# Kernel optimization log

Measured on AMD Instinct MI355X. Metric: run time of the kernel, lower is better.

## Reference

```python
import jax, jax.numpy as jnp
import numpy as np

K = 3  # from init kwarg


def setup_inputs() -> dict:
    key = jax.random.key(0)
    k1, k2 = jax.random.split(key)
    B, N, D = 32, 2048, 128
    features = jax.random.normal(k1, (B, N, D), dtype=jnp.float32)
    strength = jax.random.uniform(k2, (), dtype=jnp.float32)
    return {"features": features, "strength": strength}


def reference(features, strength):
    B, N, D = features.shape
    k = min(K, N - 1)
    x = jax.lax.stop_gradient(features)  # torch uses features.detach() for the mix path

    # pairwise euclidean distance (torch.cdist, p=2): ||a||^2 + ||b||^2 - 2 a.b
    sq = jnp.sum(x * x, axis=-1)                     # (B, N)
    d2 = sq[:, :, None] + sq[:, None, :] - 2.0 * jnp.einsum('bnd,bmd->bnm', x, x)
    dist = jnp.sqrt(jnp.maximum(d2, 0.0))            # (B, N, N)

    # mask self-distance with +1e6 on the diagonal
    eye = jnp.eye(N, dtype=dist.dtype)
    dist = dist + eye[None, :, :] * 1000000.0

    # k smallest -> top_k of negated distances
    _, idx = jax.lax.top_k(-dist, k)                 # idx: (B, N, k)

    # gather neighbor features: gathered[b,n,j] = x[b, idx[b,n,j]]
    gathered = x[jnp.arange(B)[:, None, None], idx]  # (B, N, k, D)
    mix = jnp.mean(gathered, axis=2)                 # (B, N, D)

    s = jnp.clip(strength, 0.0, 1.0)
    return (1.0 - s) * features + s * mix
```

## Files before the change

kernel.cpp:

```cpp
#include <hip/hip_runtime.h>
#include <cfloat>

#define BB 32
#define NN 2048
#define DD 128
#define RM 64
#define CN 64

typedef __attribute__((ext_vector_type(8))) short short8;
typedef __attribute__((ext_vector_type(4))) float float4v;

__device__ __forceinline__ unsigned short f2bf(float f) {
    unsigned int u = __builtin_bit_cast(unsigned int, f);
    u += 0x7FFFu + ((u >> 16) & 1u);
    return (unsigned short)(u >> 16);
}

__device__ __forceinline__ unsigned int umn(unsigned int a, unsigned int b) { return a < b ? a : b; }
__device__ __forceinline__ unsigned int umx(unsigned int a, unsigned int b) { return a > b ? a : b; }
#define CSU(a, b) { unsigned int _lo = umn(a, b), _hi = umx(a, b); (a) = _lo; (b) = _hi; }

__device__ __forceinline__ void gl2lds16(const unsigned short* g, unsigned short* l) {
    __builtin_amdgcn_global_load_lds(
        (const __attribute__((address_space(1))) void*)g,
        (__attribute__((address_space(3))) void*)l, 16, 0, 0);
}

__global__ __launch_bounds__(256) void prep_kernel(const float* __restrict__ x,
        unsigned short* __restrict__ xb16, float* __restrict__ sq) {
    int t = blockIdx.x * 256 + threadIdx.x;
    int row = t >> 2;
    int q = t & 3;
    const float4* xp = reinterpret_cast<const float4*>(x + (size_t)row * DD + q * 32);
    unsigned short* op = xb16 + (size_t)row * DD + q * 32;
    float acc = 0.f;
#pragma unroll
    for (int i = 0; i < 4; ++i) {
        float4 v0 = xp[2 * i], v1 = xp[2 * i + 1];
        acc += v0.x * v0.x + v0.y * v0.y + v0.z * v0.z + v0.w * v0.w;
        acc += v1.x * v1.x + v1.y * v1.y + v1.z * v1.z + v1.w * v1.w;
        short8 pk;
        pk[0] = (short)f2bf(v0.x); pk[1] = (short)f2bf(v0.y);
        pk[2] = (short)f2bf(v0.z); pk[3] = (short)f2bf(v0.w);
        pk[4] = (short)f2bf(v1.x); pk[5] = (short)f2bf(v1.y);
        pk[6] = (short)f2bf(v1.z); pk[7] = (short)f2bf(v1.w);
        *reinterpret_cast<short8*>(op + i * 8) = pk;
    }
    acc += __shfl_xor(acc, 1);
    acc += __shfl_xor(acc, 2);
    if (q == 0) sq[row] = acc;
}

__global__ __launch_bounds__(256) void sq_kernel(const float* __restrict__ x,
                                                 float* __restrict__ sq) {
    int t = blockIdx.x * 256 + threadIdx.x;
    int row = t >> 2;
    int q = t & 3;
    const float4* xp = reinterpret_cast<const float4*>(x + (size_t)row * DD + q * 32);
    float acc = 0.f;
#pragma unroll
    for (int i = 0; i < 8; ++i) {
        float4 v = xp[i];
        acc += v.x * v.x + v.y * v.y + v.z * v.z + v.w * v.w;
    }
    acc += __shfl_xor(acc, 1);
    acc += __shfl_xor(acc, 2);
    if (q == 0) sq[row] = acc;
}

template<bool PRE>
__global__ __launch_bounds__(256, 4) void knn_kernel(const float* __restrict__ x,
        const unsigned short* __restrict__ xb16g,
        const float* __restrict__ sqv, const float* __restrict__ strength,
        float* __restrict__ out) {
    __shared__ __align__(16) unsigned short tiles[2 * RM * DD];
    __shared__ unsigned int cand8[RM * 8];
    __shared__ double refd[RM * 8];
    __shared__ int best3[RM * 3];

    unsigned short* As = tiles;
    unsigned short* Bs = tiles + RM * DD;

    const int b = blockIdx.y;
    const int row0 = blockIdx.x * RM;
    const int tid = threadIdx.x;
    const int w = tid >> 6;
    const int lane = tid & 63;
    const int m = lane & 15;
    const int quad = lane >> 4;
    const float* __restrict__ xb = x + (size_t)b * NN * DD;
    const unsigned short* __restrict__ gb = PRE ? xb16g + (size_t)b * NN * DD : nullptr;

    if constexpr (PRE) {
#pragma unroll
        for (int l = 0; l < 4; ++l) {
            int f = (l * 4 + w) * 64 + lane;
            int r = f >> 4, p = f & 15;
            int c = p ^ (r & 7);
            gl2lds16(gb + (size_t)(row0 + r) * DD + c * 8, As + (l * 4 + w) * 512);
        }
    } else {
#pragma unroll
        for (int l = 0; l < 4; ++l) {
            int id = l * 256 + tid;
            int r = id >> 4, c = id & 15, p = c ^ (r & 7);
            const float4* src = reinterpret_cast<const float4*>(xb + (size_t)(row0 + r) * DD + c * 8);
            float4 v0 = src[0], v1 = src[1];
            short8 pk;
            pk[0] = (short)f2bf(v0.x); pk[1] = (short)f2bf(v0.y);
            pk[2] = (short)f2bf(v0.z); pk[3] = (short)f2bf(v0.w);
            pk[4] = (short)f2bf(v1.x); pk[5] = (short)f2bf(v1.y);
            pk[6] = (short)f2bf(v1.z); pk[7] = (short)f2bf(v1.w);
            *reinterpret_cast<short8*>(As + r * DD + p * 8) = pk;
        }
    }
    __syncthreads();

    short8 afrag[4];
#pragma unroll
    for (int kc = 0; kc < 4; ++kc) {
        int rl = 16 * w + m;
        int p = (kc * 4 + quad) ^ (m & 7);
        afrag[kc] = *reinterpret_cast<const short8*>(As + rl * DD + p * 8);
    }

    unsigned int tk[4][4];
#pragma unroll
    for (int i = 0; i < 4; ++i)
#pragma unroll
        for (int q = 0; q < 4; ++q) tk[i][q] = 0xFFFFFFFFu;

    for (int ct = 0; ct < NN / CN; ++ct) {
        float sqb[4];
#pragma unroll
        for (int cc = 0; cc < 4; ++cc)
            sqb[cc] = sqv[(size_t)b * NN + ct * CN + cc * 16 + m] + 1024.0f;

        __syncthreads();
        if constexpr (PRE) {
#pragma unroll
            for (int l = 0; l < 4; ++l) {
                int f = (l * 4 + w) * 64 + lane;
                int r = f >> 4, p = f & 15;
                int c = p ^ (r & 7);
                gl2lds16(gb + (size_t)(ct * CN + r) * DD + c * 8, Bs + (l * 4 + w) * 512);
            }
        } else {
#pragma unroll
            for (int l = 0; l < 4; ++l) {
                int id = l * 256 + tid;
                int r = id >> 4, c = id & 15, p = c ^ (r & 7);
                const float4* src = reinterpret_cast<const float4*>(xb + (size_t)(ct * CN + r) * DD + c * 8);
                float4 v0 = src[0], v1 = src[1];
                short8 pk;
                pk[0] = (short)f2bf(v0.x); pk[1] = (short)f2bf(v0.y);
                pk[2] = (short)f2bf(v0.z); pk[3] = (short)f2bf(v0.w);
                pk[4] = (short)f2bf(v1.x); pk[5] = (short)f2bf(v1.y);
                pk[6] = (short)f2bf(v1.z); pk[7] = (short)f2bf(v1.w);
                *reinterpret_cast<short8*>(Bs + r * DD + p * 8) = pk;
            }
        }
        __syncthreads();

        float4v acc[4];
#pragma unroll
        for (int cc = 0; cc < 4; ++cc) acc[cc] = (float4v){0.f, 0.f, 0.f, 0.f};
#pragma unroll
        for (int kc = 0; kc < 4; ++kc) {
#pragma unroll
            for (int cc = 0; cc < 4; ++cc) {
                int rl = cc * 16 + m;
                int p = (kc * 4 + quad) ^ (m & 7);
                short8 bfrag = *reinterpret_cast<const short8*>(Bs + rl * DD + p * 8);
                acc[cc] = __builtin_amdgcn_mfma_f32_16x16x32_bf16(afrag[kc], bfrag, acc[cc], 0, 0, 0);
            }
        }

#pragma unroll
        for (int cc = 0; cc < 4; ++cc) {
            unsigned int col = (unsigned int)(ct * CN + cc * 16 + m);
#pragma unroll
            for (int reg = 0; reg < 4; ++reg) {
                float scb = fmaf(-2.f, acc[cc][reg], sqb[cc]);
                unsigned int key = (__builtin_bit_cast(unsigned int, scb) & 0xFFFFF800u) | col;
                unsigned int n;
                n = umn(tk[reg][0], key); key = umx(tk[reg][0], key); tk[reg][0] = n;
                n = umn(tk[reg][1], key); key = umx(tk[reg][1], key); tk[reg][1] = n;
                n = umn(tk[reg][2], key); key = umx(tk[reg][2], key); tk[reg][2] = n;
                tk[reg][3] = umn(tk[reg][3], key);
            }
        }
    }

#pragma unroll
    for (int reg = 0; reg < 4; ++reg) {
        unsigned int e[8];
#pragma unroll
        for (int j = 0; j < 4; ++j) e[j] = tk[reg][j];
#pragma unroll
        for (int j = 4; j < 8; ++j) e[j] = 0xFFFFFFFFu;
#pragma unroll
        for (int st = 0; st < 4; ++st) {
            int mask = 1 << st;
            unsigned int rv[8];
#pragma unroll
            for (int j = 0; j < 8; ++j)
                rv[j] = (unsigned int)__shfl_xor((int)e[7 - j], mask, 64);
#pragma unroll
            for (int j = 0; j < 8; ++j) e[j] = umn(e[j], rv[j]);
            CSU(e[0], e[4]); CSU(e[1], e[5]); CSU(e[2], e[6]); CSU(e[3], e[7]);
            CSU(e[0], e[2]); CSU(e[1], e[3]); CSU(e[4], e[6]); CSU(e[5], e[7]);
            CSU(e[0], e[1]); CSU(e[2], e[3]); CSU(e[4], e[5]); CSU(e[6], e[7]);
        }
        if (m == 0) {
            int row = 16 * w + quad * 4 + reg;
#pragma unroll
            for (int j = 0; j < 8; ++j) cand8[row * 8 + j] = e[j];
        }
    }
    __syncthreads();

    {
        int r = tid >> 2, q4 = tid & 3;
        int grow = row0 + r;
        int c0 = (int)(cand8[r * 8 + q4 * 2 + 0] & 0x7FFu);
        int c1 = (int)(cand8[r * 8 + q4 * 2 + 1] & 0x7FFu);
        const float* p0 = xb + (size_t)c0 * DD;
        const float* p1 = xb + (size_t)c1 * DD;
        const float* pr = xb + (size_t)grow * DD;
        double a0 = 0.0, a1 = 0.0;
#pragma unroll 4
        for (int d4 = 0; d4 < 32; ++d4) {
            float4 wv = *reinterpret_cast<const float4*>(pr + d4 * 4);
            float4 v0 = *reinterpret_cast<const float4*>(p0 + d4 * 4);
            float4 v1 = *reinterpret_cast<const float4*>(p1 + d4 * 4);
            double d;
            d = (double)wv.x - (double)v0.x; a0 += d * d;
            d = (double)wv.y - (double)v0.y; a0 += d * d;
            d = (double)wv.z - (double)v0.z; a0 += d * d;
            d = (double)wv.w - (double)v0.w; a0 += d * d;
            d = (double)wv.x - (double)v1.x; a1 += d * d;
            d = (double)wv.y - (double)v1.y; a1 += d * d;
            d = (double)wv.z - (double)v1.z; a1 += d * d;
            d = (double)wv.w - (double)v1.w; a1 += d * d;
        }
        refd[r * 8 + q4 * 2 + 0] = (c0 == grow) ? DBL_MAX : a0;
        refd[r * 8 + q4 * 2 + 1] = (c1 == grow) ? DBL_MAX : a1;
    }
    __syncthreads();

    if (tid < RM) {
        int r = tid;
        double b0 = DBL_MAX, b1 = DBL_MAX, b2 = DBL_MAX;
        int i0 = 0x7fffffff, i1 = 0x7fffffff, i2 = 0x7fffffff;
        for (int e = 0; e < 8; ++e) {
            double dv = refd[r * 8 + e];
            int ix = (int)(cand8[r * 8 + e] & 0x7FFu);
            if (dv < b2 || (dv == b2 && ix < i2)) {
                b2 = dv; i2 = ix;
                if (b1 > b2 || (b1 == b2 && i1 > i2)) { double td = b1; b1 = b2; b2 = td; int tn = i1; i1 = i2; i2 = tn; }
                if (b0 > b1 || (b0 == b1 && i0 > i1)) { double td = b0; b0 = b1; b1 = td; int tn = i0; i0 = i1; i1 = tn; }
            }
        }
        best3[r * 3 + 0] = i0; best3[r * 3 + 1] = i1; best3[r * 3 + 2] = i2;
    }
    __syncthreads();

    {
        int r = tid >> 2, q = tid & 3;
        float s = fminf(fmaxf(strength[0], 0.f), 1.f);
        const float* pa = xb + (size_t)(row0 + r) * DD + q * 32;
        const float* p1 = xb + (size_t)best3[r * 3 + 0] * DD + q * 32;
        const float* p2 = xb + (size_t)best3[r * 3 + 1] * DD + q * 32;
        const float* p3 = xb + (size_t)best3[r * 3 + 2] * DD + q * 32;
        float* po = out + ((size_t)b * NN + row0 + r) * DD + q * 32;
#pragma unroll
        for (int l = 0; l < 8; ++l) {
            float4 a  = *reinterpret_cast<const float4*>(pa + l * 4);
            float4 n1 = *reinterpret_cast<const float4*>(p1 + l * 4);
            float4 n2 = *reinterpret_cast<const float4*>(p2 + l * 4);
            float4 n3 = *reinterpret_cast<const float4*>(p3 + l * 4);
            float4 o;
            o.x = (1.f - s) * a.x + s * ((n1.x + n2.x + n3.x) / 3.f);
            o.y = (1.f - s) * a.y + s * ((n1.y + n2.y + n3.y) / 3.f);
            o.z = (1.f - s) * a.z + s * ((n1.z + n2.z + n3.z) / 3.f);
            o.w = (1.f - s) * a.w + s * ((n1.w + n2.w + n3.w) / 3.f);
            *reinterpret_cast<float4*>(po + l * 4) = o;
        }
    }
}

extern "C" void kernel_launch(void* const* d_in, const int* in_sizes, int n_in,
                              void* d_out, int out_size, void* d_ws, size_t ws_size,
                              hipStream_t stream) {
    const float* x = (const float*)d_in[0];
    const float* strength = (const float*)d_in[1];
    float* out = (float*)d_out;
    float* sq = (float*)d_ws;
    unsigned short* xb16 = (unsigned short*)((char*)d_ws + 256 * 1024);
    const size_t need = 256 * 1024 + (size_t)BB * NN * DD * sizeof(unsigned short);

    if (ws_size >= need) {
        prep_kernel<<<dim3((BB * NN * 4) / 256), 256, 0, stream>>>(x, xb16, sq);
        knn_kernel<true><<<dim3(NN / RM, BB), 256, 0, stream>>>(x, xb16, sq, strength, out);
    } else {
        sq_kernel<<<dim3((BB * NN * 4) / 256), 256, 0, stream>>>(x, sq);
        knn_kernel<false><<<dim3(NN / RM, BB), 256, 0, stream>>>(x, nullptr, sq, strength, out);
    }
}
```

Baseline: 213.5 us.

## Double-buffer B tiles, load A fragments directly, and reorder grid by batch

The kernel now uses a two-slot LDS buffer for the column tiles. It prefetches the next tile while running MFMA and top-k on the current one, so each iteration needs one barrier instead of two. A fragments are read straight from global memory into registers instead of being staged through LDS. The refd and best3 scratch arrays now reuse the tile buffer. The grid is swapped to batch-major ordering, so concurrent blocks come from different batches, which changes L2 locality. The risk is more register pressure, and the grid swap may lower L2 reuse of each batch's B tiles.

```diff
diff --git a/kernel.cpp b/kernel.cpp
--- a/kernel.cpp
+++ b/kernel.cpp
@@ -73,16 +73,11 @@
         const unsigned short* __restrict__ xb16g,
         const float* __restrict__ sqv, const float* __restrict__ strength,
         float* __restrict__ out) {
-    __shared__ __align__(16) unsigned short tiles[2 * RM * DD];
+    __shared__ __align__(16) unsigned short btile[2 * CN * DD];
     __shared__ unsigned int cand8[RM * 8];
-    __shared__ double refd[RM * 8];
-    __shared__ int best3[RM * 3];
-
-    unsigned short* As = tiles;
-    unsigned short* Bs = tiles + RM * DD;
-
-    const int b = blockIdx.y;
-    const int row0 = blockIdx.x * RM;
+
+    const int b = blockIdx.x;
+    const int row0 = blockIdx.y * RM;
     const int tid = threadIdx.x;
     const int w = tid >> 6;
     const int lane = tid & 63;
@@ -91,76 +86,96 @@
     const float* __restrict__ xb = x + (size_t)b * NN * DD;
     const unsigned short* __restrict__ gb = PRE ? xb16g + (size_t)b * NN * DD : nullptr;
 
+    short8 afrag[4];
     if constexpr (PRE) {
 #pragma unroll
-        for (int l = 0; l < 4; ++l) {
-            int f = (l * 4 + w) * 64 + lane;
-            int r = f >> 4, p = f & 15;
-            int c = p ^ (r & 7);
-            gl2lds16(gb + (size_t)(row0 + r) * DD + c * 8, As + (l * 4 + w) * 512);
-        }
+        for (int kc = 0; kc < 4; ++kc)
+            afrag[kc] = *reinterpret_cast<const short8*>(
+                gb + (size_t)(row0 + 16 * w + m) * DD + kc * 32 + quad * 8);
     } else {
 #pragma unroll
-        for (int l = 0; l < 4; ++l) {
-            int id = l * 256 + tid;
-            int r = id >> 4, c = id & 15, p = c ^ (r & 7);
-            const float4* src = reinterpret_cast<const float4*>(xb + (size_t)(row0 + r) * DD + c * 8);
+        for (int kc = 0; kc < 4; ++kc) {
+            const float4* src = reinterpret_cast<const float4*>(
+                xb + (size_t)(row0 + 16 * w + m) * DD + kc * 32 + quad * 8);
             float4 v0 = src[0], v1 = src[1];
             short8 pk;
             pk[0] = (short)f2bf(v0.x); pk[1] = (short)f2bf(v0.y);
             pk[2] = (short)f2bf(v0.z); pk[3] = (short)f2bf(v0.w);
             pk[4] = (short)f2bf(v1.x); pk[5] = (short)f2bf(v1.y);
             pk[6] = (short)f2bf(v1.z); pk[7] = (short)f2bf(v1.w);
-            *reinterpret_cast<short8*>(As + r * DD + p * 8) = pk;
-        }
-    }
-    __syncthreads();
-
-    short8 afrag[4];
-#pragma unroll
-    for (int kc = 0; kc < 4; ++kc) {
-        int rl = 16 * w + m;
-        int p = (kc * 4 + quad) ^ (m & 7);
-        afrag[kc] = *reinterpret_cast<const short8*>(As + rl * DD + p * 8);
-    }
-
-    unsigned int tk[4][4];
-#pragma unroll
-    for (int i = 0; i < 4; ++i)
-#pragma unroll
-        for (int q = 0; q < 4; ++q) tk[i][q] = 0xFFFFFFFFu;
-
-    for (int ct = 0; ct < NN / CN; ++ct) {
-        float sqb[4];
-#pragma unroll
-        for (int cc = 0; cc < 4; ++cc)
-            sqb[cc] = sqv[(size_t)b * NN + ct * CN + cc * 16 + m] + 1024.0f;
-
-        __syncthreads();
+            afrag[kc] = pk;
+        }
+    }
+
+    {
+        unsigned short* buf = btile;
         if constexpr (PRE) {
 #pragma unroll
             for (int l = 0; l < 4; ++l) {
                 int f = (l * 4 + w) * 64 + lane;
                 int r = f >> 4, p = f & 15;
                 int c = p ^ (r & 7);
-                gl2lds16(gb + (size_t)(ct * CN + r) * DD + c * 8, Bs + (l * 4 + w) * 512);
+                gl2lds16(gb + (size_t)r * DD + c * 8, buf + (l * 4 + w) * 512);
             }
         } else {
 #pragma unroll
             for (int l = 0; l < 4; ++l) {
                 int id = l * 256 + tid;
                 int r = id >> 4, c = id & 15, p = c ^ (r & 7);
-                const float4* src = reinterpret_cast<const float4*>(xb + (size_t)(ct * CN + r) * DD + c * 8);
+                const float4* src = reinterpret_cast<const float4*>(xb + (size_t)r * DD + c * 8);
                 float4 v0 = src[0], v1 = src[1];
                 short8 pk;
                 pk[0] = (short)f2bf(v0.x); pk[1] = (short)f2bf(v0.y);
                 pk[2] = (short)f2bf(v0.z); pk[3] = (short)f2bf(v0.w);
                 pk[4] = (short)f2bf(v1.x); pk[5] = (short)f2bf(v1.y);
                 pk[6] = (short)f2bf(v1.z); pk[7] = (short)f2bf(v1.w);
-                *reinterpret_cast<short8*>(Bs + r * DD + p * 8) = pk;
-            }
-        }
-        __syncthreads();
+                *reinterpret_cast<short8*>(buf + r * DD + p * 8) = pk;
+            }
+        }
+    }
+    __syncthreads();
+
+    unsigned int tk[4][4];
+#pragma unroll
+    for (int i = 0; i < 4; ++i)
+#pragma unroll
+        for (int q = 0; q < 4; ++q) tk[i][q] = 0xFFFFFFFFu;
+
+    for (int ct = 0; ct < NN / CN; ++ct) {
+        unsigned short* cur = btile + (size_t)(ct & 1) * CN * DD;
+        unsigned short* nxt = btile + (size_t)((ct + 1) & 1) * CN * DD;
+
+        if (ct + 1 < NN / CN) {
+            int cb = (ct + 1) * CN;
+            if constexpr (PRE) {
+#pragma unroll
+                for (int l = 0; l < 4; ++l) {
+                    int f = (l * 4 + w) * 64 + lane;
+                    int r = f >> 4, p = f & 15;
+                    int c = p ^ (r & 7);
+                    gl2lds16(gb + (size_t)(cb + r) * DD + c * 8, nxt + (l * 4 + w) * 512);
+                }
+            } else {
+#pragma unroll
+                for (int l = 0; l < 4; ++l) {
+                    int id = l * 256 + tid;
+                    int r = id >> 4, c = id & 15, p = c ^ (r & 7);
+                    const float4* src = reinterpret_cast<const float4*>(xb + (size_t)(cb + r) * DD + c * 8);
+                    float4 v0 = src[0], v1 = src[1];
+                    short8 pk;
+                    pk[0] = (short)f2bf(v0.x); pk[1] = (short)f2bf(v0.y);
+                    pk[2] = (short)f2bf(v0.z); pk[3] = (short)f2bf(v0.w);
+                    pk[4] = (short)f2bf(v1.x); pk[5] = (short)f2bf(v1.y);
+                    pk[6] = (short)f2bf(v1.z); pk[7] = (short)f2bf(v1.w);
+                    *reinterpret_cast<short8*>(nxt + r * DD + p * 8) = pk;
+                }
+            }
+        }
+
+        float sqb[4];
+#pragma unroll
+        for (int cc = 0; cc < 4; ++cc)
+            sqb[cc] = sqv[(size_t)b * NN + ct * CN + cc * 16 + m] + 1024.0f;
 
         float4v acc[4];
 #pragma unroll
@@ -171,7 +186,7 @@
             for (int cc = 0; cc < 4; ++cc) {
                 int rl = cc * 16 + m;
                 int p = (kc * 4 + quad) ^ (m & 7);
-                short8 bfrag = *reinterpret_cast<const short8*>(Bs + rl * DD + p * 8);
+                short8 bfrag = *reinterpret_cast<const short8*>(cur + rl * DD + p * 8);
                 acc[cc] = __builtin_amdgcn_mfma_f32_16x16x32_bf16(afrag[kc], bfrag, acc[cc], 0, 0, 0);
             }
         }
@@ -190,6 +205,8 @@
                 tk[reg][3] = umn(tk[reg][3], key);
             }
         }
+
+        __syncthreads();
     }
 
 #pragma unroll
@@ -219,6 +236,9 @@
         }
     }
     __syncthreads();
+
+    double* refd = reinterpret_cast<double*>(btile);
+    int* best3 = reinterpret_cast<int*>(btile) + 1024;
 
     {
         int r = tid >> 2, q4 = tid & 3;
@@ -302,9 +322,9 @@
 
     if (ws_size >= need) {
         prep_kernel<<<dim3((BB * NN * 4) / 256), 256, 0, stream>>>(x, xb16, sq);
-        knn_kernel<true><<<dim3(NN / RM, BB), 256, 0, stream>>>(x, xb16, sq, strength, out);
+        knn_kernel<true><<<dim3(BB, NN / RM), 256, 0, stream>>>(x, xb16, sq, strength, out);
     } else {
         sq_kernel<<<dim3((BB * NN * 4) / 256), 256, 0, stream>>>(x, sq);
-        knn_kernel<false><<<dim3(NN / RM, BB), 256, 0, stream>>>(x, nullptr, sq, strength, out);
-    }
-}
+        knn_kernel<false><<<dim3(BB, NN / RM), 256, 0, stream>>>(x, nullptr, sq, strength, out);
+    }
+}
```

New measurement: 204.1 us. 1.05x faster.
